# Kernel optimization log

Measured on AMD Instinct MI355X. Metric: run time of the kernel, lower is better.

The kernel has to match this reference:

```python
import jax, jax.numpy as jnp
import numpy as np


def _cdist(p, t):
    # p: [N,3], t: [N,3] -> euclidean distance matrix [N,N] (torch.cdist p=2)
    d2 = (jnp.sum(p * p, -1)[:, None] + jnp.sum(t * t, -1)[None, :]
          - 2.0 * (p @ t.T))
    return jnp.sqrt(jnp.maximum(d2, 1e-12))


def _greedy_match_cost(cost):
    # cost: [N,N]. For each row i in order, pick the cheapest unused column.
    N = cost.shape[0]

    def step(used, row):
        masked = jnp.where(used, jnp.inf, row)
        j = jnp.argmin(masked)
        c = masked[j]
        return used.at[j].set(True), c

    _, per_point_cost = jax.lax.scan(step, jnp.zeros(N, dtype=bool), cost)
    return jnp.mean(per_point_cost)


def setup_inputs() -> dict:
    key = jax.random.key(0)
    k1, k2 = jax.random.split(key)
    B, N = 8, 2048
    pred = jax.random.normal(k1, (B, N, 3), dtype=jnp.float32)
    target = jax.random.normal(k2, (B, N, 3), dtype=jnp.float32)
    return {"pred": pred, "target": target}


def reference(pred, target):
    # cost matrices per batch: [B,N,N]
    cost = jax.vmap(_cdist)(pred, target)
    emd = jax.vmap(_greedy_match_cost)(cost)  # [B]
    return jnp.mean(emd)
```

## Files before the change

kernel.cpp:

```cpp
#include <hip/hip_runtime.h>

#define NPTS 2048
#define TOPK 32
#define RPB  8

typedef float v2f __attribute__((ext_vector_type(2)));
typedef unsigned int u32;
typedef u32 v2u __attribute__((ext_vector_type(2)));
typedef unsigned long long u64;

static __device__ __forceinline__ u32 umin32(u32 a, u32 b) { return b < a ? b : a; }
static __device__ __forceinline__ u64 umin64(u64 a, u64 b) { return b < a ? b : a; }

template <int CTRL>
static __device__ __forceinline__ u32 dpp_min(u32 m) {
  return umin32(m, (u32)__builtin_amdgcn_mov_dpp((int)m, CTRL, 0xF, 0xF, true));
}
static __device__ __forceinline__ u32 x16_min(u32 m) {
#if __has_builtin(__builtin_amdgcn_permlane16_swap)
  auto r = __builtin_amdgcn_permlane16_swap((int)m, (int)m, false, false);
  return umin32(m, umin32((u32)r[0], (u32)r[1]));
#else
  return umin32(m, (u32)__builtin_amdgcn_ds_swizzle((int)m, 0x401F));
#endif
}
static __device__ __forceinline__ u32 x32_min(u32 m) {
#if __has_builtin(__builtin_amdgcn_permlane32_swap)
  auto r = __builtin_amdgcn_permlane32_swap((int)m, (int)m, false, false);
  return umin32(m, umin32((u32)r[0], (u32)r[1]));
#else
  return umin32(m, (u32)__shfl_xor((int)m, 32, 64));
#endif
}
static __device__ __forceinline__ u32 sext_bit(u32 mask, int c) {
#if __has_builtin(__builtin_amdgcn_sbfe)
  return (u32)__builtin_amdgcn_sbfe((int)mask, c, 1);
#else
  return (u32)(((int)(mask << (31 - c))) >> 31);
#endif
}

template <int CTRL>
static __device__ __forceinline__ u64 dpp_min64(u64 k) {
  unsigned lo = (unsigned)k, hi = (unsigned)(k >> 32);
  unsigned olo = (unsigned)__builtin_amdgcn_mov_dpp((int)lo, CTRL, 0xF, 0xF, true);
  unsigned ohi = (unsigned)__builtin_amdgcn_mov_dpp((int)hi, CTRL, 0xF, 0xF, true);
  return umin64(k, ((u64)ohi << 32) | olo);
}
static __device__ __forceinline__ u64 x16_min64(u64 k) {
  unsigned lo = (unsigned)k, hi = (unsigned)(k >> 32);
#if __has_builtin(__builtin_amdgcn_permlane16_swap)
  auto rlo = __builtin_amdgcn_permlane16_swap(lo, lo, false, false);
  auto rhi = __builtin_amdgcn_permlane16_swap(hi, hi, false, false);
  u64 a = ((u64)rhi[0] << 32) | rlo[0];
  u64 b = ((u64)rhi[1] << 32) | rlo[1];
  return umin64(k, umin64(a, b));
#else
  unsigned olo = (unsigned)__builtin_amdgcn_ds_swizzle((int)lo, 0x401F);
  unsigned ohi = (unsigned)__builtin_amdgcn_ds_swizzle((int)hi, 0x401F);
  return umin64(k, ((u64)ohi << 32) | olo);
#endif
}
static __device__ __forceinline__ u64 x32_min64(u64 k) {
  unsigned lo = (unsigned)k, hi = (unsigned)(k >> 32);
#if __has_builtin(__builtin_amdgcn_permlane32_swap)
  auto rlo = __builtin_amdgcn_permlane32_swap(lo, lo, false, false);
  auto rhi = __builtin_amdgcn_permlane32_swap(hi, hi, false, false);
  u64 a = ((u64)rhi[0] << 32) | rlo[0];
  u64 b = ((u64)rhi[1] << 32) | rlo[1];
  return umin64(k, umin64(a, b));
#else
  unsigned olo = (unsigned)__shfl_xor((int)lo, 32, 64);
  unsigned ohi = (unsigned)__shfl_xor((int)hi, 32, 64);
  return umin64(k, ((u64)ohi << 32) | olo);
#endif
}
static __device__ __forceinline__ u64 wave_min_u64(u64 k) {
  k = dpp_min64<0xB1>(k);
  k = dpp_min64<0x4E>(k);
  k = dpp_min64<0x141>(k);
  k = dpp_min64<0x140>(k);
  k = x16_min64(k);
  k = x32_min64(k);
  return k;
}

#define FOR16(M) M(0) M(1) M(2) M(3) M(4) M(5) M(6) M(7) \
                 M(8) M(9) M(10) M(11) M(12) M(13) M(14) M(15)

#define LOADP(h) \
  v2f TX##h, TY##h, TZ##h, TQ##h; \
  { float x0 = tb[6*h+0], y0 = tb[6*h+1], z0 = tb[6*h+2]; \
    float x1 = tb[6*h+3], y1 = tb[6*h+4], z1 = tb[6*h+5]; \
    TX##h = (v2f){x0, x1}; TY##h = (v2f){y0, y1}; TZ##h = (v2f){z0, z1}; \
    TQ##h = (v2f){x0*x0 + y0*y0 + z0*z0, x1*x1 + y1*y1 + z1*z1}; }

#define DISTK(h) u64 KA##h, KB##h; { \
  v2f dot = __builtin_elementwise_fma(TX##h, Xv, \
              __builtin_elementwise_fma(TY##h, Yv, TZ##h * Zv)); \
  v2f dd  = __builtin_elementwise_fma(m2v, dot, TQ##h); \
  v2f d2  = Qv + dd; \
  float c0 = fmaxf(d2.x, 1e-12f), c1 = fmaxf(d2.y, 1e-12f); \
  KA##h = ((u64)(u32)__float_as_int(c0) << 32) | (u32)(base + 2*(h)); \
  KB##h = ((u64)(u32)__float_as_int(c1) << 32) | (u32)(base + 2*(h) + 1); }

#define G4(a, b, c, d) umin64(umin64(a, b), umin64(c, d))
#define ZG(c, KV, RL) case (c): KV = own ? ~0ULL : KV; goto RL;

__global__ __launch_bounds__(64, 2) void emd_topk_kernel(
    const float* __restrict__ pred, const float* __restrict__ target,
    u64* __restrict__ lists) {
  const int blk = blockIdx.x;
  const int b  = blk / (NPTS / RPB);
  const int r0 = (blk % (NPTS / RPB)) * RPB;
  const int lane = threadIdx.x;
  const float* p = pred + (size_t)b * NPTS * 3;
  const float* t = target + (size_t)b * NPTS * 3;

  const float* tb = t + (size_t)lane * 32 * 3;
  FOR16(LOADP)
  const int base = lane << 5;
  const v2f m2v = {-2.f, -2.f};

#pragma unroll 1
  for (int rr = 0; rr < RPB; ++rr) {
    const int i = r0 + rr;
    const float X = p[3 * i], Y = p[3 * i + 1], Z = p[3 * i + 2];
    const float Q = fmaf(X, X, fmaf(Y, Y, Z * Z));
    const v2f Xv = {X, X}, Yv = {Y, Y}, Zv = {Z, Z}, Qv = {Q, Q};
    FOR16(DISTK)

    u64 g0 = G4(KA0, KB0, KA1, KB1),   g1 = G4(KA2, KB2, KA3, KB3);
    u64 g2 = G4(KA4, KB4, KA5, KB5),   g3 = G4(KA6, KB6, KA7, KB7);
    u64 g4 = G4(KA8, KB8, KA9, KB9),   g5 = G4(KA10, KB10, KA11, KB11);
    u64 g6 = G4(KA12, KB12, KA13, KB13), g7 = G4(KA14, KB14, KA15, KB15);
    u64 h0 = umin64(g0, g1), h1 = umin64(g2, g3);
    u64 h2 = umin64(g4, g5), h3 = umin64(g6, g7);
    u64 q0 = umin64(h0, h1), q1 = umin64(h2, h3);
    u64 root = umin64(q0, q1);

    u64* out = lists + ((size_t)b * NPTS + i) * TOPK;
#pragma unroll 1
    for (int e = 0; e < TOPK; ++e) {
      u64 m = wave_min_u64(root);
      if (lane == 0) out[e] = m;
      if (e == TOPK - 1) break;
      const u32 col = (u32)m & (u32)(NPTS - 1);
      const bool own = (lane == (int)(col >> 5));
      const u32 k5 = col & 31u;
      switch (k5) {
        ZG(0,  KA0,  R0) ZG(1,  KB0,  R0) ZG(2,  KA1,  R0) ZG(3,  KB1,  R0)
        ZG(4,  KA2,  R1) ZG(5,  KB2,  R1) ZG(6,  KA3,  R1) ZG(7,  KB3,  R1)
        ZG(8,  KA4,  R2) ZG(9,  KB4,  R2) ZG(10, KA5,  R2) ZG(11, KB5,  R2)
        ZG(12, KA6,  R3) ZG(13, KB6,  R3) ZG(14, KA7,  R3) ZG(15, KB7,  R3)
        ZG(16, KA8,  R4) ZG(17, KB8,  R4) ZG(18, KA9,  R4) ZG(19, KB9,  R4)
        ZG(20, KA10, R5) ZG(21, KB10, R5) ZG(22, KA11, R5) ZG(23, KB11, R5)
        ZG(24, KA12, R6) ZG(25, KB12, R6) ZG(26, KA13, R6) ZG(27, KB13, R6)
        ZG(28, KA14, R7) ZG(29, KB14, R7) ZG(30, KA15, R7) ZG(31, KB15, R7)
        default: __builtin_unreachable();
      }
      R0: g0 = G4(KA0, KB0, KA1, KB1);     h0 = umin64(g0, g1); q0 = umin64(h0, h1); root = umin64(q0, q1); continue;
      R1: g1 = G4(KA2, KB2, KA3, KB3);     h0 = umin64(g0, g1); q0 = umin64(h0, h1); root = umin64(q0, q1); continue;
      R2: g2 = G4(KA4, KB4, KA5, KB5);     h1 = umin64(g2, g3); q0 = umin64(h0, h1); root = umin64(q0, q1); continue;
      R3: g3 = G4(KA6, KB6, KA7, KB7);     h1 = umin64(g2, g3); q0 = umin64(h0, h1); root = umin64(q0, q1); continue;
      R4: g4 = G4(KA8, KB8, KA9, KB9);     h2 = umin64(g4, g5); q1 = umin64(h2, h3); root = umin64(q0, q1); continue;
      R5: g5 = G4(KA10, KB10, KA11, KB11); h2 = umin64(g4, g5); q1 = umin64(h2, h3); root = umin64(q0, q1); continue;
      R6: g6 = G4(KA12, KB12, KA13, KB13); h3 = umin64(g6, g7); q1 = umin64(h2, h3); root = umin64(q0, q1); continue;
      R7: g7 = G4(KA14, KB14, KA15, KB15); h3 = umin64(g6, g7); q1 = umin64(h2, h3); root = umin64(q0, q1); continue;
    }
  }
}


#define LD16(M) M(0) M(1) M(2) M(3) M(4) M(5) M(6) M(7) \
                M(8) M(9) M(10) M(11) M(12) M(13) M(14) M(15)
#define DECLA(j) uint4 A##j;
#define LDA(j)   A##j = Lr[j];
#define WRC(j)   { cl64w[(2*(j)) * 64 + lane]     = ((u64)A##j.y << 32) | A##j.x; \
                   cl64w[(2*(j) + 1) * 64 + lane] = ((u64)A##j.w << 32) | A##j.z; }
#define FREEB(j) { \
    u32 c0 = A##j.x & 2047u, c1 = A##j.z & 2047u; \
    u32 w0 = sbm[c0 >> 5], w1 = sbm[c1 >> 5]; \
    alive |= ((~(w0 >> (c0 & 31u))) & 1u) << (2*(j)); \
    alive |= ((~(w1 >> (c1 & 31u))) & 1u) << (2*(j)+1); }

__global__ __launch_bounds__(64, 1) void emd_seq_kernel(
    const float* __restrict__ pred, const float* __restrict__ target,
    const u64* __restrict__ lists, float* __restrict__ batch_sums) {
  const int b = blockIdx.x, lane = threadIdx.x;
  const float* t = target + (size_t)b * NPTS * 3;
  const float* p = pred + (size_t)b * NPTS * 3;

  __shared__ float4 tt[NPTS];
  __shared__ u64 cl64s[TOPK * 64];
  __shared__ u32 claim[NPTS];
  __shared__ u32 fl[NPTS];
  __shared__ u32 sbitmap[64];
  __shared__ float4 ppred[64];

  for (int j = lane; j < NPTS; j += 64) {
    float x = t[3 * j], y = t[3 * j + 1], z = t[3 * j + 2];
    tt[((j & 31) << 6) | ((j >> 5) ^ (j & 31))] =
        make_float4(x, y, z, fmaf(x, x, fmaf(y, y, z * z)));
  }
  sbitmap[lane] = 0u;
  __syncthreads();

  const u64* L = lists + (size_t)b * NPTS * TOPK;
  u64* cl64w = cl64s;
  const u64* cl64 = cl64s;
  volatile u32* sbm = sbitmap;
  volatile u32* vclaim = claim;
  float psum = 0.f;

  const uint4* Lr = (const uint4*)(L + (size_t)lane * TOPK);
  LD16(DECLA)
  LD16(LDA)

#pragma unroll 1
  for (int blk = 0; blk < NPTS / 64; ++blk) {
    LD16(WRC)
    u32 alive = 0u;
    LD16(FREEB)
    { const float* pr = p + (size_t)(blk * 64 + lane) * 3;
      float X = pr[0], Y = pr[1], Z = pr[2];
      ppred[lane] = make_float4(X, Y, Z, fmaf(X, X, fmaf(Y, Y, Z * Z))); }
    { int nrow = (blk + 1) * 64 + lane; nrow = nrow < NPTS ? nrow : NPTS - 1;
      Lr = (const uint4*)(L + (size_t)nrow * TOPK); }
    LD16(LDA)
#pragma unroll
    for (int k = 0; k < 32; ++k) claim[k * 64 + lane] = ~0u;

    bool committed = false;
    bool exh = (alive == 0u);
    u32 rank = 0, col = 0;
    u64 cur = 0;
    if (!exh) {
      rank = (u32)__ffs(alive) - 1u;
      cur = cl64[rank * 64 + lane];
      col = (u32)cur & 2047u;
      atomicMin(&claim[col], (u32)lane);
    }
    bool flBuilt = false;
    u32 F = 0;

    int oguard = 0;
#pragma unroll 1
    while (true) {
      int guard = 0;
      while (true) {
        bool changed = false;
        if (!committed && !exh) {
          int g2 = 0;
          while (true) {
            u32 c = vclaim[col];
            if (c >= (u32)lane) break;
            alive &= ~(1u << rank);
            if (alive == 0u) { exh = true; break; }
            rank = (u32)__ffs(alive) - 1u;
            cur = cl64[rank * 64 + lane];
            col = (u32)cur & 2047u;
            atomicMin(&claim[col], (u32)lane);
            changed = true;
            if (++g2 > 33) break;
          }
        }
        if (__ballot(changed) == 0ULL) break;
        if (++guard > 3000) break;
      }

      u64 exbl = __ballot(exh && !committed);
      if (exbl == 0ULL) break;
      int rstar = __ffsll(exbl) - 1;

      if (!committed && !exh && lane < rstar) {
        atomicOr(&sbitmap[col >> 5], 1u << (col & 31u));
        psum += sqrtf(__uint_as_float((u32)(cur >> 32)));
        committed = true;
      }

      if (!flBuilt) {
        u32 fw = ~sbm[lane];
        u32 cnt = __popc(fw);
        u32 pfx = cnt;
#pragma unroll
        for (int d = 1; d < 64; d <<= 1) {
          u32 o = (u32)__shfl_up((int)pfx, d, 64);
          if (lane >= d) pfx += o;
        }
        F = (u32)__shfl((int)pfx, 63, 64);
        pfx -= cnt;
        while (fw) {
          int bpos = __ffs(fw) - 1;
          fw &= fw - 1u;
          fl[pfx++] = ((u32)lane << 5) + (u32)bpos;
        }
        flBuilt = true;
      }

      {
        float4 P4 = ppred[rstar];
        float X = P4.x, Y = P4.y, Z = P4.z, Q = P4.w;
        u64 mb = ~0ULL;
        for (u32 k = (u32)lane; k < F; k += 64) {
          u32 c = fl[k];
          u32 used = (sbm[c >> 5] >> (c & 31u)) & 1u;
          float4 c4 = tt[((c & 31u) << 6) | ((c >> 5) ^ (c & 31u))];
          float dot = fmaf(c4.x, X, fmaf(c4.y, Y, c4.z * Z));
          float d2 = Q + fmaf(-2.f, dot, c4.w);
          d2 = fmaxf(d2, 1e-12f);
          u64 kk = ((u64)(u32)__float_as_int(d2) << 32) | c;
          if (used) kk = ~0ULL;
          mb = umin64(mb, kk);
        }
        mb = wave_min_u64(mb);
        u32 cst = (u32)mb & 2047u;
        if (lane == rstar) {
          psum += sqrtf(__uint_as_float((u32)(mb >> 32)));
          committed = true;
          atomicOr(&sbitmap[cst >> 5], 1u << (cst & 31u));
          atomicMin(&claim[cst], (u32)rstar);
        }
      }
      if (++oguard > 66) break;
    }

    if (!committed) {
      atomicOr(&sbitmap[col >> 5], 1u << (col & 31u));
      psum += sqrtf(__uint_as_float((u32)(cur >> 32)));
    }
  }

  float v = psum;
  v += __shfl_xor(v, 1, 64);
  v += __shfl_xor(v, 2, 64);
  v += __shfl_xor(v, 4, 64);
  v += __shfl_xor(v, 8, 64);
  v += __shfl_xor(v, 16, 64);
  v += __shfl_xor(v, 32, 64);
  if (lane == 0) batch_sums[b] = v;
}

#define DECLRU(h) v2u RU##h;
#define DIST(h) { \
  v2f dot = __builtin_elementwise_fma(TX##h, Xv, \
              __builtin_elementwise_fma(TY##h, Yv, TZ##h * Zv)); \
  v2f dd  = __builtin_elementwise_fma(m2v, dot, TQ##h); \
  v2f d2  = Qv + dd; \
  RU##h = (v2u){(u32)__float_as_int(d2.x), (u32)__float_as_int(d2.y)}; }
#define TOUR(h, c) { \
  u32 u0 = RU##h.x | sext_bit(usedmask, 2*h); \
  u32 u1 = RU##h.y | sext_bit(usedmask, 2*h + 1); \
  u32 pu = umin32(u0, u1); \
  u32 pk = (u1 < u0) ? (u32)(2*h + 1) : (u32)(2*h); \
  if (pu < bc##c) { bc##c = pu; kc##c = pk; } }

__global__ __launch_bounds__(64, 1) void emd_greedy_kernel(
    const float* __restrict__ pred, const float* __restrict__ target,
    float* __restrict__ batch_sums) {
  const int b = blockIdx.x, lane = threadIdx.x;
  const float* p = pred + (size_t)b * NPTS * 3;
  const float* t = target + (size_t)b * NPTS * 3;
  __shared__ float4 pp[NPTS + 2];
  for (int i = lane; i < NPTS; i += 64) {
    float x = p[3 * i], y = p[3 * i + 1], z = p[3 * i + 2];
    pp[i] = make_float4(x, y, z, x * x + y * y + z * z);
  }
  if (lane < 2) pp[NPTS + lane] = make_float4(0.f, 0.f, 0.f, 0.f);
  const float* tb = t + (size_t)lane * 32 * 3;
  FOR16(LOADP)
  FOR16(DECLRU)
  u32 usedmask = 0;
  float sum = 0.f;
  __syncthreads();
  const v2f m2v = {-2.f, -2.f};
  v2f Xv, Yv, Zv, Qv;
  {
    float4 A = pp[0];
    Xv = (v2f){A.x, A.x}; Yv = (v2f){A.y, A.y};
    Zv = (v2f){A.z, A.z}; Qv = (v2f){A.w, A.w};
    FOR16(DIST)
  }
  for (int i = 0; i < NPTS; ++i) {
    float4 An = pp[i + 1];
    u32 bc0 = ~0u, bc1 = ~0u, bc2 = ~0u, bc3 = ~0u;
    u32 kc0 = 0, kc1 = 0, kc2 = 0, kc3 = 0;
    TOUR(0, 0)  TOUR(1, 0)  TOUR(2, 0)  TOUR(3, 0)
    TOUR(4, 1)  TOUR(5, 1)  TOUR(6, 1)  TOUR(7, 1)
    TOUR(8, 2)  TOUR(9, 2)  TOUR(10, 2) TOUR(11, 2)
    TOUR(12, 3) TOUR(13, 3) TOUR(14, 3) TOUR(15, 3)
    bool s01 = bc1 < bc0; u32 v01 = s01 ? bc1 : bc0; u32 i01 = s01 ? kc1 : kc0;
    bool s23 = bc3 < bc2; u32 v23 = s23 ? bc3 : bc2; u32 i23 = s23 ? kc3 : kc2;
    bool sf  = v23 < v01; u32 bu  = sf ? v23 : v01; u32 bk  = sf ? i23 : i01;
    Xv = (v2f){An.x, An.x}; Yv = (v2f){An.y, An.y};
    Zv = (v2f){An.z, An.z}; Qv = (v2f){An.w, An.w};
    FOR16(DIST)
    u32 m = bu;
    m = dpp_min<0xB1>(m); m = dpp_min<0x4E>(m);
    m = dpp_min<0x141>(m); m = dpp_min<0x140>(m);
    m = x16_min(m); m = x32_min(m);
    u64 mk = __ballot(bu == m);
    int first = __ffsll(mk) - 1;
    usedmask |= (lane == first) ? (1u << bk) : 0u;
    sum += sqrtf(fmaxf(__uint_as_float(m), 1e-12f));
  }
  if (lane == 0) batch_sums[b] = sum;
}

__global__ void emd_finalize_kernel(const float* __restrict__ batch_sums,
                                    float* __restrict__ out, int B) {
  float acc = 0.f;
  for (int b = 0; b < B; ++b) acc += batch_sums[b] / (float)NPTS;
  out[0] = acc / (float)B;
}

extern "C" void kernel_launch(void* const* d_in, const int* in_sizes, int n_in,
                              void* d_out, int out_size, void* d_ws, size_t ws_size,
                              hipStream_t stream) {
  const float* pred   = (const float*)d_in[0];
  const float* target = (const float*)d_in[1];
  float* out = (float*)d_out;
  const int B = in_sizes[0] / (NPTS * 3);

  const size_t need = 256 + (size_t)B * NPTS * TOPK * sizeof(u64);
  if (ws_size >= need) {
    float* bs = (float*)d_ws;
    u64* lists = (u64*)((char*)d_ws + 256);
    emd_topk_kernel<<<B * (NPTS / RPB), 64, 0, stream>>>(pred, target, lists);
    emd_seq_kernel<<<B, 64, 0, stream>>>(pred, target, lists, bs);
    emd_finalize_kernel<<<1, 1, 0, stream>>>(bs, out, B);
  } else {
    float* bs = (float*)d_ws;
    emd_greedy_kernel<<<B, 64, 0, stream>>>(pred, target, bs);
    emd_finalize_kernel<<<1, 1, 0, stream>>>(bs, out, B);
  }
}
```

Measured before the change: 461.0 us.

## Handle last 128 rows with direct scan over compacted free columns

Stops the speculative top-K block loop after 30 blocks and processes the final 128 rows with a dedicated tail. The tail compacts the remaining free columns (at most 128) into a list, holds two candidates per lane, and does an exact wave-wide argmin per row. This targets the cost of top-K list exhaustion and fallback paths that grow near the end, when most columns are used. In exchange the tail is strictly sequential, with one wave reduction per row.

```diff
diff --git a/kernel.cpp b/kernel.cpp
--- a/kernel.cpp
+++ b/kernel.cpp
@@ -3,6 +3,8 @@
 #define NPTS 2048
 #define TOPK 32
 #define RPB  8
+#define MAINBLKS 30
+#define TAILROWS (NPTS - MAINBLKS * 64)
 
 typedef float v2f __attribute__((ext_vector_type(2)));
 typedef unsigned int u32;
@@ -197,6 +199,7 @@
   __shared__ u32 fl[NPTS];
   __shared__ u32 sbitmap[64];
   __shared__ float4 ppred[64];
+  __shared__ float4 tpred[TAILROWS];
 
   for (int j = lane; j < NPTS; j += 64) {
     float x = t[3 * j], y = t[3 * j + 1], z = t[3 * j + 2];
@@ -218,7 +221,7 @@
   LD16(LDA)
 
 #pragma unroll 1
-  for (int blk = 0; blk < NPTS / 64; ++blk) {
+  for (int blk = 0; blk < MAINBLKS; ++blk) {
     LD16(WRC)
     u32 alive = 0u;
     LD16(FREEB)
@@ -331,6 +334,53 @@
     }
   }
 
+  {
+    u32 fw = ~sbm[lane];
+    u32 cnt = __popc(fw);
+    u32 pfx = cnt;
+#pragma unroll
+    for (int d = 1; d < 64; d <<= 1) {
+      u32 o = (u32)__shfl_up((int)pfx, d, 64);
+      if (lane >= d) pfx += o;
+    }
+    u32 F = (u32)__shfl((int)pfx, 63, 64);
+    pfx -= cnt;
+    while (fw) {
+      int bpos = __ffs(fw) - 1;
+      fw &= fw - 1u;
+      fl[pfx++] = ((u32)lane << 5) + (u32)bpos;
+    }
+    { const float* pr = p + (size_t)(MAINBLKS * 64 + lane) * 3;
+      float X = pr[0], Y = pr[1], Z = pr[2];
+      tpred[lane] = make_float4(X, Y, Z, fmaf(X, X, fmaf(Y, Y, Z * Z))); }
+    { const float* pr = p + (size_t)(MAINBLKS * 64 + 64 + lane) * 3;
+      float X = pr[0], Y = pr[1], Z = pr[2];
+      tpred[64 + lane] = make_float4(X, Y, Z, fmaf(X, X, fmaf(Y, Y, Z * Z))); }
+
+    bool l0 = (u32)lane < F, l1 = (u32)(64 + lane) < F;
+    u32 c0 = l0 ? fl[lane] : 0u;
+    u32 c1 = l1 ? fl[64 + lane] : 0u;
+    float4 t0 = tt[((c0 & 31u) << 6) | ((c0 >> 5) ^ (c0 & 31u))];
+    float4 t1 = tt[((c1 & 31u) << 6) | ((c1 >> 5) ^ (c1 & 31u))];
+
+#pragma unroll 1
+    for (int r = 0; r < TAILROWS; ++r) {
+      float4 P = tpred[r];
+      float X = P.x, Y = P.y, Z = P.z, Q = P.w;
+      float dot0 = fmaf(t0.x, X, fmaf(t0.y, Y, t0.z * Z));
+      float d20 = fmaxf(Q + fmaf(-2.f, dot0, t0.w), 1e-12f);
+      float dot1 = fmaf(t1.x, X, fmaf(t1.y, Y, t1.z * Z));
+      float d21 = fmaxf(Q + fmaf(-2.f, dot1, t1.w), 1e-12f);
+      u64 k0 = l0 ? (((u64)(u32)__float_as_int(d20) << 32) | c0) : ~0ULL;
+      u64 k1 = l1 ? (((u64)(u32)__float_as_int(d21) << 32) | c1) : ~0ULL;
+      u64 k = wave_min_u64(umin64(k0, k1));
+      u32 wc = (u32)k & 2047u;
+      l0 = l0 && (c0 != wc);
+      l1 = l1 && (c1 != wc);
+      if (lane == 0) psum += sqrtf(__uint_as_float((u32)(k >> 32)));
+    }
+  }
+
   float v = psum;
   v += __shfl_xor(v, 1, 64);
   v += __shfl_xor(v, 2, 64);
```

After: 408.4 us. 11.4% less time.
